# Performance work log

Hardware: AMD Instinct MI355X
Metric: run time of the kernel (lower is better)

Reference implementation:

```python
import jax, jax.numpy as jnp
import numpy as np

B, K, D, DH, GH = 4096, 16384, 512, 512, 32
MAX_ITER = 30
TOL = 1e-5

def setup_inputs() -> dict:
    key = jax.random.key(0)
    k = jax.random.split(key, 7)
    s = lambda fan: 1.0 / np.sqrt(fan)  # torch nn.Linear default init scale
    return {
        "query": jax.random.normal(k[0], (B, D), jnp.float32),
        "patterns": jax.random.normal(k[1], (K, D), jnp.float32),
        "Wq": jax.random.uniform(k[2], (D, DH), jnp.float32, -s(D), s(D)),
        "Wk": jax.random.uniform(k[3], (D, DH), jnp.float32, -s(D), s(D)),
        "Wv": jax.random.uniform(k[4], (D, D), jnp.float32, -s(D), s(D)),
        "log_beta": jnp.log(jnp.asarray(2.0, jnp.float32)),  # beta_init=2.0
        "g1_w": jax.random.uniform(k[5], (2 * D + 1, GH), jnp.float32, -s(2 * D + 1), s(2 * D + 1)),
        "g1_b": jnp.zeros((GH,), jnp.float32),
        "g2_w": jax.random.uniform(k[6], (GH, 1), jnp.float32, -s(GH), s(GH)),
        "g2_b": jnp.zeros((1,), jnp.float32),
    }

def _attn_step(z, Wq, k_projT, v_proj, beta):
    # z: (B, d) -> softmax(beta * (zWq)(KWk)^T) @ (KWv): (B, d)
    logits = beta * ((z @ Wq) @ k_projT)  # (B, K)
    return jax.nn.softmax(logits, axis=-1) @ v_proj

def reference(query, patterns, Wq, Wk, Wv, log_beta, g1_w, g1_b, g2_w, g2_b):
    beta = jnp.exp(log_beta)
    k_projT = (patterns @ Wk).T  # (dh, K)
    v_proj = patterns @ Wv       # (K, d)

    # shallow path: one attention step from the raw query
    out_shallow = _attn_step(query, Wq, k_projT, v_proj, beta)

    # deep path: fixed-point iteration z = f(z), z0 = out_shallow
    def cond(c):
        _, rel, it = c
        return (rel > TOL) & (it < MAX_ITER)

    def body(c):
        z, _, it = c
        z_new = _attn_step(z, Wq, k_projT, v_proj, beta)
        rel = jnp.linalg.norm(z_new - z) / (jnp.linalg.norm(z_new) + 1e-8)
        return z_new, rel, it + 1

    out_deep, _, _ = jax.lax.while_loop(cond, body, (out_shallow, jnp.float32(1.0), 0))

    # gate on [shallow, deep, ||shallow - deep||]
    div = jnp.linalg.norm(out_shallow - out_deep, axis=-1, keepdims=True)  # (B, 1)
    gate_in = jnp.concatenate([out_shallow, out_deep, div], axis=-1)       # (B, 2d+1)
    h = jax.nn.gelu(gate_in @ g1_w + g1_b, approximate=False)  # torch GELU is exact erf
    alpha = jax.nn.sigmoid(h @ g2_w + g2_b)                    # (B, 1)
    output = alpha * out_shallow + (1.0 - alpha) * out_deep
    return output, out_shallow, out_deep
```

## Files before the change

### kernel.cpp

```cpp
#include <hip/hip_runtime.h>
#include <hip/hip_bf16.h>
#include <math.h>

#define BROWS 4096
#define KPAT  16384
#define DDIM  512
#define NGRP  256
#define TOLF  1e-5f
#define KSEGS 8
#define KSEGLEN (KPAT / KSEGS)

typedef __attribute__((ext_vector_type(8))) short bf16x8;
typedef __attribute__((ext_vector_type(8))) _Float16 f16x8;
typedef __attribute__((ext_vector_type(4))) float f32x4;

typedef __attribute__((address_space(1))) const void gvoid_t;
typedef __attribute__((address_space(3))) void lvoid_t;
#define ASYNC_COPY16(g, l) \
  __builtin_amdgcn_global_load_lds((gvoid_t*)(g), (lvoid_t*)(l), 16, 0, 0)

#define SWZ_SCOL(lane) ((((lane) & 7) ^ (((lane) >> 3) & 7)) * 8)
#define SWZ_OFF(R, G)  (((R) * 64) + ((((G) ^ ((R) & 7))) * 8))

__device__ __forceinline__ unsigned short f2bf_rn(float x) {
  unsigned u = __float_as_uint(x);
  u = u + 0x7FFFu + ((u >> 16) & 1u);
  return (unsigned short)(u >> 16);
}
__device__ __forceinline__ unsigned short f2h_bits(float x) {
  union { _Float16 h; unsigned short u; } cv;
  cv.h = (_Float16)x;
  return cv.u;
}
__device__ __forceinline__ float h_bits2f(unsigned short u) {
  union { _Float16 h; unsigned short u; } cv;
  cv.u = u;
  return (float)cv.h;
}

__global__ void init_kernel(float* acc, int* flag) {
  acc[0] = 0.f; acc[1] = 0.f;
  acc[2] = 1e30f;
  *flag = 0;
}

__global__ void zero_out_kernel(float* p, int n, const int* __restrict__ flag) {
  if (flag && *(volatile const int*)flag) return;
  int i = blockIdx.x * 256 + threadIdx.x;
  if (i < n) p[i] = 0.f;
}

__global__ __launch_bounds__(256) void transpose_kernel(
    const float* __restrict__ in, void* __restrict__ outp,
    int R, int C, int ldO, int coff, int mode)
{
  __shared__ float tile[32][33];
  const int bx = blockIdx.x, by = blockIdx.y;
  const int tx = threadIdx.x & 31, ty = threadIdx.x >> 5;
  #pragma unroll
  for (int j = 0; j < 4; ++j) {
    int rr = by * 32 + ty + j * 8;
    tile[ty + j * 8][tx] = in[(long)rr * C + bx * 32 + tx];
  }
  __syncthreads();
  #pragma unroll
  for (int j = 0; j < 4; ++j) {
    int orow = bx * 32 + ty + j * 8;
    int ocol = by * 32 + tx;
    float v = tile[tx][ty + j * 8];
    if (mode == 2) ((unsigned short*)outp)[(long)orow * ldO + coff + ocol] = f2h_bits(v);
    else           ((float*)outp)[(long)orow * ldO + coff + ocol] = v;
  }
}

__global__ __launch_bounds__(256) void pack_split(
    const float* __restrict__ X, unsigned short* __restrict__ Y, int n)
{
  int i = blockIdx.x * 256 + threadIdx.x;
  if (i >= n) return;
  float x = X[i];
  unsigned u = __float_as_uint(x);
  unsigned short hi = (unsigned short)(u >> 16);
  float hif = __uint_as_float(u & 0xFFFF0000u);
  unsigned short lo = f2bf_rn(x - hif);
  int r = i >> 9, c = i & 511;
  Y[(long)r * 1024 + c] = hi;
  Y[(long)r * 1024 + 512 + c] = lo;
}

__global__ __launch_bounds__(256) void pack_f16(
    const float* __restrict__ X, unsigned short* __restrict__ Y, int n)
{
  int i = blockIdx.x * 256 + threadIdx.x;
  if (i >= n) return;
  Y[i] = f2h_bits(X[i]);
}

__global__ __launch_bounds__(256) void btgemm_setup(
    const unsigned short* __restrict__ A,
    const unsigned short* __restrict__ Bm,
    float* __restrict__ C, int ldC)
{
  __shared__ unsigned short As[128 * 64];
  __shared__ unsigned short Bs[128 * 64];
  const int tid = threadIdx.x;
  const int w = tid >> 6, lane = tid & 63;
  const int wm = w >> 1, wn = w & 1;
  const long mBase = (long)blockIdx.y * 128;
  const long nBase = (long)blockIdx.x * 128;

  f32x4 acc[4][4];
  const f32x4 zero4 = {0.f, 0.f, 0.f, 0.f};
  #pragma unroll
  for (int i = 0; i < 4; ++i)
    #pragma unroll
    for (int j = 0; j < 4; ++j) acc[i][j] = zero4;

  const int srow = w * 32 + (lane >> 3);
  const int scol = SWZ_SCOL(lane);
  const unsigned short* Ag = A + (mBase + srow) * 1024L + scol;
  const unsigned short* Bg = Bm + (nBase + srow) * 1024L + scol;
  unsigned short* AsW = As + w * 2048;
  unsigned short* BsW = Bs + w * 2048;
  const int lrow = lane & 15, lkq = lane >> 4;
  const int rx = lrow & 7;

  for (int k0 = 0; k0 < 1536; k0 += 64) {
    const int ak = (k0 < 512)  ? k0 : k0 - 512;
    const int bk = (k0 < 1024) ? k0 : k0 - 1024;
    __syncthreads();
    #pragma unroll
    for (int j = 0; j < 4; ++j) {
      ASYNC_COPY16(Ag + (long)j * 8 * 1024 + ak, AsW + j * 512);
      ASYNC_COPY16(Bg + (long)j * 8 * 1024 + bk, BsW + j * 512);
    }
    __syncthreads();
    #pragma unroll
    for (int s = 0; s < 2; ++s) {
      bf16x8 af[4], bfv[4];
      #pragma unroll
      for (int mi = 0; mi < 4; ++mi)
        af[mi] = *(const bf16x8*)(As + (wm * 64 + mi * 16 + lrow) * 64
                                     + (((s * 4 + lkq) ^ rx) * 8));
      #pragma unroll
      for (int ni = 0; ni < 4; ++ni)
        bfv[ni] = *(const bf16x8*)(Bs + (wn * 64 + ni * 16 + lrow) * 64
                                      + (((s * 4 + lkq) ^ rx) * 8));
      #pragma unroll
      for (int mi = 0; mi < 4; ++mi)
        #pragma unroll
        for (int ni = 0; ni < 4; ++ni)
          acc[mi][ni] = __builtin_amdgcn_mfma_f32_16x16x32_bf16(af[mi], bfv[ni], acc[mi][ni], 0, 0, 0);
    }
  }

  const int r0 = lkq * 4, cc = lrow;
  #pragma unroll
  for (int mi = 0; mi < 4; ++mi)
    #pragma unroll
    for (int r = 0; r < 4; ++r) {
      const long grow = mBase + wm * 64 + mi * 16 + r0 + r;
      #pragma unroll
      for (int ni = 0; ni < 4; ++ni) {
        const long gcol = nBase + wn * 64 + ni * 16 + cc;
        C[grow * ldC + gcol] = acc[mi][ni][r];
      }
    }
}

__global__ __launch_bounds__(256) void btgemm_exp(
    const unsigned short* __restrict__ A,
    const unsigned short* __restrict__ Bm,
    unsigned short* __restrict__ P,
    float* __restrict__ smax, float* __restrict__ ssum,
    const float* __restrict__ log_beta,
    const int* __restrict__ flag)
{
  if (flag && *(volatile const int*)flag) return;
  __shared__ unsigned short As[128 * 64];
  __shared__ unsigned short Bs[128 * 64];
  const float beta = __expf(log_beta[0]);
  const int tid = threadIdx.x;
  const int w = tid >> 6, lane = tid & 63;
  const int wm = w >> 1, wn = w & 1;
  const long mBase = (long)blockIdx.x * 128;
  const long nBase = (long)blockIdx.y * 128;

  f32x4 acc[4][4];
  const f32x4 zero4 = {0.f, 0.f, 0.f, 0.f};
  #pragma unroll
  for (int i = 0; i < 4; ++i)
    #pragma unroll
    for (int j = 0; j < 4; ++j) acc[i][j] = zero4;

  const int srow = w * 32 + (lane >> 3);
  const int scol = SWZ_SCOL(lane);
  const unsigned short* Ag = A + (mBase + srow) * 512L + scol;
  const unsigned short* Bg = Bm + (nBase + srow) * 512L + scol;
  unsigned short* AsW = As + w * 2048;
  unsigned short* BsW = Bs + w * 2048;
  const int lrow = lane & 15, lkq = lane >> 4;
  const int rx = lrow & 7;

  for (int k0 = 0; k0 < 512; k0 += 64) {
    __syncthreads();
    #pragma unroll
    for (int j = 0; j < 4; ++j) {
      ASYNC_COPY16(Ag + (long)j * 8 * 512 + k0, AsW + j * 512);
      ASYNC_COPY16(Bg + (long)j * 8 * 512 + k0, BsW + j * 512);
    }
    __syncthreads();
    #pragma unroll
    for (int s = 0; s < 2; ++s) {
      f16x8 af[4], bfv[4];
      #pragma unroll
      for (int mi = 0; mi < 4; ++mi)
        af[mi] = *(const f16x8*)(As + (wm * 64 + mi * 16 + lrow) * 64
                                    + (((s * 4 + lkq) ^ rx) * 8));
      #pragma unroll
      for (int ni = 0; ni < 4; ++ni)
        bfv[ni] = *(const f16x8*)(Bs + (wn * 64 + ni * 16 + lrow) * 64
                                     + (((s * 4 + lkq) ^ rx) * 8));
      #pragma unroll
      for (int mi = 0; mi < 4; ++mi)
        #pragma unroll
        for (int ni = 0; ni < 4; ++ni)
          acc[mi][ni] = __builtin_amdgcn_mfma_f32_16x16x32_f16(af[mi], bfv[ni], acc[mi][ni], 0, 0, 0);
    }
  }

  const int r0 = lkq * 4, cc = lrow;
  const int g = (int)(nBase >> 6) + wn;
  const long gbase = nBase + wn * 64;
  #pragma unroll
  for (int mi = 0; mi < 4; ++mi) {
    #pragma unroll
    for (int r = 0; r < 4; ++r) {
      const long grow = mBase + wm * 64 + mi * 16 + r0 + r;
      float rm = fmaxf(fmaxf(acc[mi][0][r], acc[mi][1][r]),
                       fmaxf(acc[mi][2][r], acc[mi][3][r]));
      #pragma unroll
      for (int off = 1; off < 16; off <<= 1)
        rm = fmaxf(rm, __shfl_xor(rm, off, 64));
      unsigned short pv[4];
      float se = 0.f;
      #pragma unroll
      for (int ni = 0; ni < 4; ++ni) {
        pv[ni] = f2h_bits(__expf(beta * (acc[mi][ni][r] - rm)));
        se += h_bits2f(pv[ni]);
      }
      #pragma unroll
      for (int ni = 0; ni < 4; ++ni)
        P[grow * KPAT + gbase + ni * 16 + cc] = pv[ni];
      #pragma unroll
      for (int off = 1; off < 16; off <<= 1)
        se += __shfl_xor(se, off, 64);
      if (cc == 0) {
        smax[grow * NGRP + g] = rm;
        ssum[grow * NGRP + g] = se;
      }
    }
  }
}

__global__ __launch_bounds__(256) void scale_kernel(
    const float* __restrict__ smax, const float* __restrict__ ssum,
    float* __restrict__ tvec, float* __restrict__ lbuf,
    const float* __restrict__ log_beta, const int* __restrict__ flag)
{
  if (flag && *(volatile const int*)flag) return;
  const int row = blockIdx.x, tid = threadIdx.x;
  const float beta = __expf(log_beta[0]);
  __shared__ float red[8];
  __shared__ float M_s;
  float m = smax[(long)row * NGRP + tid];
  float mm = m;
  #pragma unroll
  for (int off = 32; off >= 1; off >>= 1) mm = fmaxf(mm, __shfl_down(mm, off, 64));
  if ((tid & 63) == 0) red[tid >> 6] = mm;
  __syncthreads();
  if (tid == 0) M_s = fmaxf(fmaxf(red[0], red[1]), fmaxf(red[2], red[3]));
  __syncthreads();
  const float M = M_s;
  const float t = __expf(beta * (m - M));
  tvec[(long)row * NGRP + tid] = t;
  float lp = t * ssum[(long)row * NGRP + tid];
  #pragma unroll
  for (int off = 32; off >= 1; off >>= 1) lp += __shfl_down(lp, off, 64);
  if ((tid & 63) == 0) red[tid >> 6] = lp;
  __syncthreads();
  if (tid == 0) lbuf[row] = (red[0] + red[1]) + (red[2] + red[3]);
}

__global__ __launch_bounds__(256) void btgemm_splitk(
    const unsigned short* __restrict__ A,
    const unsigned short* __restrict__ Bm,
    const float* __restrict__ tvec,
    float* __restrict__ C,
    const int* __restrict__ flag)
{
  if (*(volatile const int*)flag) return;
  __shared__ unsigned short As[128 * 64];
  __shared__ unsigned short Bs[128 * 64];
  __shared__ float ts[128 * 33];
  const int tid = threadIdx.x;
  const int w = tid >> 6, lane = tid & 63;
  const int wm = w >> 1, wn = w & 1;
  const long mBase = (long)blockIdx.y * 128;
  const long nBase = (long)blockIdx.x * 128;
  const int kbase = blockIdx.z * KSEGLEN;
  const int g0 = kbase >> 6;

  for (int idx = tid; idx < 128 * 32; idx += 256) {
    int rr = idx >> 5, jj = idx & 31;
    ts[rr * 33 + jj] = tvec[(mBase + rr) * (long)NGRP + g0 + jj];
  }

  f32x4 acc[4][4];
  const f32x4 zero4 = {0.f, 0.f, 0.f, 0.f};
  #pragma unroll
  for (int i = 0; i < 4; ++i)
    #pragma unroll
    for (int j = 0; j < 4; ++j) acc[i][j] = zero4;

  const int srow = w * 32 + (lane >> 3);
  const int scol = SWZ_SCOL(lane);
  const unsigned short* Ag = A + (mBase + srow) * (long)KPAT + scol + kbase;
  const unsigned short* Bg = Bm + (nBase + srow) * (long)KPAT + scol + kbase;
  unsigned short* AsW = As + w * 2048;
  unsigned short* BsW = Bs + w * 2048;
  const int lrow = lane & 15, lkq = lane >> 4;
  const int rx = lrow & 7;

  for (int k0 = 0; k0 < KSEGLEN; k0 += 64) {
    __syncthreads();
    #pragma unroll
    for (int j = 0; j < 4; ++j) {
      ASYNC_COPY16(Ag + (long)j * 8 * KPAT + k0, AsW + j * 512);
      ASYNC_COPY16(Bg + (long)j * 8 * KPAT + k0, BsW + j * 512);
    }
    __syncthreads();
    const int jj = k0 >> 6;
    _Float16 th[4];
    #pragma unroll
    for (int mi = 0; mi < 4; ++mi)
      th[mi] = (_Float16)ts[(wm * 64 + mi * 16 + lrow) * 33 + jj];
    #pragma unroll
    for (int s = 0; s < 2; ++s) {
      f16x8 af[4], bfv[4];
      #pragma unroll
      for (int mi = 0; mi < 4; ++mi) {
        af[mi] = *(const f16x8*)(As + (wm * 64 + mi * 16 + lrow) * 64
                                    + (((s * 4 + lkq) ^ rx) * 8));
        f16x8 tv = {th[mi], th[mi], th[mi], th[mi], th[mi], th[mi], th[mi], th[mi]};
        af[mi] = af[mi] * tv;
      }
      #pragma unroll
      for (int ni = 0; ni < 4; ++ni)
        bfv[ni] = *(const f16x8*)(Bs + (wn * 64 + ni * 16 + lrow) * 64
                                     + (((s * 4 + lkq) ^ rx) * 8));
      #pragma unroll
      for (int mi = 0; mi < 4; ++mi)
        #pragma unroll
        for (int ni = 0; ni < 4; ++ni)
          acc[mi][ni] = __builtin_amdgcn_mfma_f32_16x16x32_f16(af[mi], bfv[ni], acc[mi][ni], 0, 0, 0);
    }
  }

  const int r0 = lkq * 4, cc = lrow;
  #pragma unroll
  for (int mi = 0; mi < 4; ++mi)
    #pragma unroll
    for (int r = 0; r < 4; ++r) {
      const long grow = mBase + wm * 64 + mi * 16 + r0 + r;
      #pragma unroll
      for (int ni = 0; ni < 4; ++ni) {
        const long gcol = nBase + wn * 64 + ni * 16 + cc;
        atomicAdd(&C[grow * DDIM + gcol], acc[mi][ni][r]);
      }
    }
}

__global__ __launch_bounds__(256) void reduce_commit(
    float4* __restrict__ zc, const float4* __restrict__ zn,
    unsigned short* __restrict__ zf16, const float* __restrict__ lvec,
    float* __restrict__ acc, const int* __restrict__ flag)
{
  if (*(volatile const int*)flag) return;
  const int tid = threadIdx.x;
  const int i = blockIdx.x * 256 + tid;
  const int row = i >> 7;
  const int c0 = (i & 127) * 4;
  const float rs = 1.0f / lvec[row];
  float4 a = zn[i];
  a.x *= rs; a.y *= rs; a.z *= rs; a.w *= rs;
  float4 b = zc[i];
  float dx = a.x - b.x, dy = a.y - b.y, dz = a.z - b.z, dw = a.w - b.w;
  float d2 = dx * dx + dy * dy + dz * dz + dw * dw;
  float n2 = a.x * a.x + a.y * a.y + a.z * a.z + a.w * a.w;
  zc[i] = a;
  *(ushort4*)(zf16 + (long)row * 512 + c0) =
      make_ushort4(f2h_bits(a.x), f2h_bits(a.y), f2h_bits(a.z), f2h_bits(a.w));

  __shared__ float rd[8], rn[8];
  #pragma unroll
  for (int off = 32; off >= 1; off >>= 1) {
    d2 += __shfl_down(d2, off, 64);
    n2 += __shfl_down(n2, off, 64);
  }
  if ((tid & 63) == 0) { rd[tid >> 6] = d2; rn[tid >> 6] = n2; }
  __syncthreads();
  if (tid == 0) {
    atomicAdd(acc,     (rd[0] + rd[1]) + (rd[2] + rd[3]));
    atomicAdd(acc + 1, (rn[0] + rn[1]) + (rn[2] + rn[3]));
  }
}

__global__ __launch_bounds__(256) void commit_shallow(
    float4* __restrict__ shal, float4* __restrict__ zc,
    const float4* __restrict__ zn, unsigned short* __restrict__ zf16,
    const float* __restrict__ lvec)
{
  const int i = blockIdx.x * 256 + threadIdx.x;
  const int row = i >> 7;
  const int c0 = (i & 127) * 4;
  const float rs = 1.0f / lvec[row];
  float4 a = zn[i];
  a.x *= rs; a.y *= rs; a.z *= rs; a.w *= rs;
  shal[i] = a; zc[i] = a;
  *(ushort4*)(zf16 + (long)row * 512 + c0) =
      make_ushort4(f2h_bits(a.x), f2h_bits(a.y), f2h_bits(a.z), f2h_bits(a.w));
}

__global__ void finalize_kernel(float* acc, int* flag) {
  if (*flag) return;
  float rel = sqrtf(acc[0]) / (sqrtf(acc[1]) + 1e-8f);
  float prev = acc[2];
  if (rel <= TOLF || (rel < 5e-3f && rel >= prev)) *flag = 1;
  acc[2] = rel;
  acc[0] = 0.f; acc[1] = 0.f;
}

__global__ __launch_bounds__(256) void epilogue_kernel(
    const float* __restrict__ shallow, const float* __restrict__ deep,
    const float* __restrict__ g1w, const float* __restrict__ g1b,
    const float* __restrict__ g2w, const float* __restrict__ g2b,
    float* __restrict__ out)
{
  const int r = blockIdx.x, tid = threadIdx.x;
  __shared__ float ss[512], sd[512], red[8], hred[8][32], hval[32];
  __shared__ float div_s, alpha_s;
  float dacc = 0.f;
  for (int c = tid; c < 512; c += 256) {
    float s = shallow[(long)r * 512 + c];
    float d = deep[(long)r * 512 + c];
    ss[c] = s; sd[c] = d;
    float df = s - d; dacc += df * df;
  }
  #pragma unroll
  for (int off = 32; off >= 1; off >>= 1) dacc += __shfl_down(dacc, off, 64);
  if ((tid & 63) == 0) red[tid >> 6] = dacc;
  __syncthreads();
  if (tid == 0) div_s = sqrtf((red[0] + red[1]) + (red[2] + red[3]));
  __syncthreads();
  const float dv = div_s;

  const int g = tid & 31, seg = tid >> 5;
  float p = 0.f;
  for (int jj = 0; jj < 64; ++jj) {
    int j = seg * 64 + jj;
    p += ss[j] * g1w[j * 32 + g] + sd[j] * g1w[(512 + j) * 32 + g];
  }
  hred[seg][g] = p;
  __syncthreads();
  if (tid < 32) {
    float h = g1b[tid] + dv * g1w[1024 * 32 + tid];
    #pragma unroll
    for (int sgi = 0; sgi < 8; ++sgi) h += hred[sgi][tid];
    float ge = 0.5f * h * (1.0f + erff(h * 0.70710678118f));
    hval[tid] = ge * g2w[tid];
  }
  __syncthreads();
  if (tid == 0) {
    float a = g2b[0];
    #pragma unroll
    for (int i = 0; i < 32; ++i) a += hval[i];
    alpha_s = 1.0f / (1.0f + expf(-a));
  }
  __syncthreads();
  const float al = alpha_s;
  const long BD = (long)BROWS * DDIM;
  for (int c = tid; c < 512; c += 256) {
    float s = ss[c], d = sd[c];
    out[(long)r * 512 + c]          = al * s + (1.f - al) * d;
    out[BD + (long)r * 512 + c]     = s;
    out[2 * BD + (long)r * 512 + c] = d;
  }
}

extern "C" void kernel_launch(void* const* d_in, const int* in_sizes, int n_in,
                              void* d_out, int out_size, void* d_ws, size_t ws_size,
                              hipStream_t stream)
{
  const float* query    = (const float*)d_in[0];
  const float* patterns = (const float*)d_in[1];
  const float* Wq       = (const float*)d_in[2];
  const float* Wk       = (const float*)d_in[3];
  const float* Wv       = (const float*)d_in[4];
  const float* log_beta = (const float*)d_in[5];
  const float* g1w      = (const float*)d_in[6];
  const float* g1b      = (const float*)d_in[7];
  const float* g2w      = (const float*)d_in[8];
  const float* g2b      = (const float*)d_in[9];
  float* out = (float*)d_out;

  char* base = (char*)d_ws;
  size_t off = 0;
  auto alloc = [&](size_t bytes) -> char* {
    char* p = base + off;
    off = (off + bytes + 255) & ~(size_t)255;
    return p;
  };
  unsigned short* At_f16 = (unsigned short*)alloc((size_t)KPAT * DDIM * 2);
  unsigned short* VPT    = (unsigned short*)alloc((size_t)DDIM * KPAT * 2);
  float* z_cur   = (float*)alloc((size_t)BROWS * DDIM * 4);
  float* z_new   = (float*)alloc((size_t)BROWS * DDIM * 4);
  float* shallow = (float*)alloc((size_t)BROWS * DDIM * 4);
  unsigned short* z_f16 = (unsigned short*)alloc((size_t)BROWS * DDIM * 2);
  float* Smax = (float*)alloc((size_t)BROWS * NGRP * 4);
  float* Ssum = (float*)alloc((size_t)BROWS * NGRP * 4);
  float* tvec = (float*)alloc((size_t)BROWS * NGRP * 4);
  float* lbuf = (float*)alloc((size_t)BROWS * 4);
  float* acc  = (float*)alloc(256);
  int* flag   = (int*)(acc + 8);
  char* scr = alloc(0);
  const size_t used = (size_t)(scr - base);
  const size_t scr_avail = (ws_size > used) ? ws_size - used : 0;

  const size_t MB = 1048576;
  const size_t MINSCR = 18 * MB;
  if (scr_avail < MINSCR) {
    zero_out_kernel<<<(out_size + 255) / 256, 256, 0, stream>>>(out, out_size, nullptr);
    return;
  }
  int c = 512;
  if      (scr_avail >= (size_t)4096 * KPAT * 2) c = 4096;
  else if (scr_avail >= (size_t)2048 * KPAT * 2) c = 2048;
  else if (scr_avail >= (size_t)1024 * KPAT * 2) c = 1024;
  const int nch = BROWS / c;

  unsigned short* P = (unsigned short*)scr;

  char* wscr = base + ((used + scr_avail - 7 * MB) & ~(size_t)255);
  unsigned short* Wk_pack  = (unsigned short*)(wscr + 0 * MB);
  unsigned short* Wq_pack  = (unsigned short*)(wscr + 1 * MB);
  unsigned short* W2T_pack = (unsigned short*)(wscr + 2 * MB);
  unsigned short* WvT_pack = (unsigned short*)(wscr + 3 * MB);
  float* W2f  = (float*)(wscr + 4 * MB);
  float* Wtmp = (float*)(wscr + 5 * MB);

  init_kernel<<<1, 1, 0, stream>>>(acc, flag);
  pack_split<<<1024, 256, 0, stream>>>(Wk, Wk_pack, 512 * 512);
  pack_split<<<1024, 256, 0, stream>>>(Wq, Wq_pack, 512 * 512);
  btgemm_setup<<<dim3(4, 4), 256, 0, stream>>>(Wk_pack, Wq_pack, W2f, 512);
  transpose_kernel<<<dim3(16, 16), 256, 0, stream>>>(W2f, Wtmp, 512, 512, 512, 0, 0);
  pack_split<<<1024, 256, 0, stream>>>(Wtmp, W2T_pack, 512 * 512);
  transpose_kernel<<<dim3(16, 16), 256, 0, stream>>>(Wv, Wtmp, 512, 512, 512, 0, 0);
  pack_split<<<1024, 256, 0, stream>>>(Wtmp, WvT_pack, 512 * 512);

  if (scr_avail >= 75 * MB) {
    unsigned short* pat_pack = (unsigned short*)scr;
    float* tmpf = (float*)(scr + (size_t)KPAT * 1024 * 2);
    pack_split<<<(KPAT * 512) / 256, 256, 0, stream>>>(patterns, pat_pack, KPAT * 512);
    btgemm_setup<<<dim3(4, KPAT / 128), 256, 0, stream>>>(pat_pack, WvT_pack, tmpf, 512);
    transpose_kernel<<<dim3(16, KPAT / 32), 256, 0, stream>>>(tmpf, VPT, KPAT, 512, KPAT, 0, 2);
    btgemm_setup<<<dim3(4, KPAT / 128), 256, 0, stream>>>(pat_pack, W2T_pack, tmpf, 512);
    pack_f16<<<(KPAT * 512) / 256, 256, 0, stream>>>(tmpf, At_f16, KPAT * 512);
  } else {
    const int pc = 1024;
    unsigned short* patc_pack = (unsigned short*)scr;
    float* tmpf = (float*)(scr + (size_t)pc * 1024 * 2);
    for (int pb = 0; pb < KPAT; pb += pc) {
      pack_split<<<pc * 2, 256, 0, stream>>>(patterns + (long)pb * 512, patc_pack, pc * 512);
      btgemm_setup<<<dim3(4, pc / 128), 256, 0, stream>>>(patc_pack, WvT_pack, tmpf, 512);
      transpose_kernel<<<dim3(16, pc / 32), 256, 0, stream>>>(tmpf, VPT, pc, 512, KPAT, pb, 2);
      btgemm_setup<<<dim3(4, pc / 128), 256, 0, stream>>>(patc_pack, W2T_pack, tmpf, 512);
      pack_f16<<<pc * 2, 256, 0, stream>>>(tmpf, At_f16 + (long)pb * 512, pc * 512);
    }
  }

  const int NZB = (BROWS * DDIM) / 256;
  const int NCB = (BROWS * DDIM / 4) / 256;

  pack_f16<<<8192, 256, 0, stream>>>(query, z_f16, BROWS * 512);
  zero_out_kernel<<<NZB, 256, 0, stream>>>(z_new, BROWS * DDIM, nullptr);
  for (int ch = 0; ch < nch; ++ch) {
    const long r0 = (long)ch * c;
    btgemm_exp<<<dim3(c / 128, 128), 256, 0, stream>>>(z_f16 + r0 * 512, At_f16, P,
                                                       Smax + r0 * NGRP, Ssum + r0 * NGRP,
                                                       log_beta, nullptr);
    scale_kernel<<<c, 256, 0, stream>>>(Smax + r0 * NGRP, Ssum + r0 * NGRP,
                                        tvec + r0 * NGRP, lbuf + r0, log_beta, nullptr);
    btgemm_splitk<<<dim3(4, c / 128, KSEGS), 256, 0, stream>>>(P, VPT, tvec + r0 * NGRP,
                                                               z_new + r0 * 512, flag);
  }
  commit_shallow<<<NCB, 256, 0, stream>>>((float4*)shallow, (float4*)z_cur,
                                          (const float4*)z_new, z_f16, lbuf);

  for (int it = 0; it < 30; ++it) {
    zero_out_kernel<<<NZB, 256, 0, stream>>>(z_new, BROWS * DDIM, flag);
    for (int ch = 0; ch < nch; ++ch) {
      const long r0 = (long)ch * c;
      btgemm_exp<<<dim3(c / 128, 128), 256, 0, stream>>>(z_f16 + r0 * 512, At_f16, P,
                                                         Smax + r0 * NGRP, Ssum + r0 * NGRP,
                                                         log_beta, flag);
      scale_kernel<<<c, 256, 0, stream>>>(Smax + r0 * NGRP, Ssum + r0 * NGRP,
                                          tvec + r0 * NGRP, lbuf + r0, log_beta, flag);
      btgemm_splitk<<<dim3(4, c / 128, KSEGS), 256, 0, stream>>>(P, VPT, tvec + r0 * NGRP,
                                                                 z_new + r0 * 512, flag);
    }
    reduce_commit<<<NCB, 256, 0, stream>>>((float4*)z_cur, (const float4*)z_new,
                                           z_f16, lbuf, acc, flag);
    finalize_kernel<<<1, 1, 0, stream>>>(acc, flag);
  }

  epilogue_kernel<<<BROWS, 256, 0, stream>>>(shallow, z_cur, g1w, g1b, g2w, g2b, out);
}
```

Measured before the change: 10.45 ms.

## Replace LDS staging with register double-buffered direct global loads in GEMMs

```diff
diff --git a/kernel.cpp b/kernel.cpp
--- a/kernel.cpp
+++ b/kernel.cpp
@@ -20,7 +20,8 @@
   __builtin_amdgcn_global_load_lds((gvoid_t*)(g), (lvoid_t*)(l), 16, 0, 0)
 
 #define SWZ_SCOL(lane) ((((lane) & 7) ^ (((lane) >> 3) & 7)) * 8)
-#define SWZ_OFF(R, G)  (((R) * 64) + ((((G) ^ ((R) & 7))) * 8))
+
+#define LD8(p) (*(const f16x8*)(p))
 
 __device__ __forceinline__ unsigned short f2bf_rn(float x) {
   unsigned u = __float_as_uint(x);
@@ -177,14 +178,16 @@
     const int* __restrict__ flag)
 {
   if (flag && *(volatile const int*)flag) return;
-  __shared__ unsigned short As[128 * 64];
-  __shared__ unsigned short Bs[128 * 64];
   const float beta = __expf(log_beta[0]);
   const int tid = threadIdx.x;
   const int w = tid >> 6, lane = tid & 63;
   const int wm = w >> 1, wn = w & 1;
   const long mBase = (long)blockIdx.x * 128;
   const long nBase = (long)blockIdx.y * 128;
+  const int lrow = lane & 15, lkq = lane >> 4;
+
+  const unsigned short* Ar = A + (mBase + wm * 64 + lrow) * 512L + lkq * 8;
+  const unsigned short* Br = Bm + (nBase + wn * 64 + lrow) * 512L + lkq * 8;
 
   f32x4 acc[4][4];
   const f32x4 zero4 = {0.f, 0.f, 0.f, 0.f};
@@ -193,39 +196,39 @@
     #pragma unroll
     for (int j = 0; j < 4; ++j) acc[i][j] = zero4;
 
-  const int srow = w * 32 + (lane >> 3);
-  const int scol = SWZ_SCOL(lane);
-  const unsigned short* Ag = A + (mBase + srow) * 512L + scol;
-  const unsigned short* Bg = Bm + (nBase + srow) * 512L + scol;
-  unsigned short* AsW = As + w * 2048;
-  unsigned short* BsW = Bs + w * 2048;
-  const int lrow = lane & 15, lkq = lane >> 4;
-  const int rx = lrow & 7;
-
-  for (int k0 = 0; k0 < 512; k0 += 64) {
-    __syncthreads();
-    #pragma unroll
-    for (int j = 0; j < 4; ++j) {
-      ASYNC_COPY16(Ag + (long)j * 8 * 512 + k0, AsW + j * 512);
-      ASYNC_COPY16(Bg + (long)j * 8 * 512 + k0, BsW + j * 512);
-    }
-    __syncthreads();
-    #pragma unroll
-    for (int s = 0; s < 2; ++s) {
-      f16x8 af[4], bfv[4];
-      #pragma unroll
-      for (int mi = 0; mi < 4; ++mi)
-        af[mi] = *(const f16x8*)(As + (wm * 64 + mi * 16 + lrow) * 64
-                                    + (((s * 4 + lkq) ^ rx) * 8));
+  f16x8 a0[4], b0[4], a1[4], b1[4];
+  #pragma unroll
+  for (int i = 0; i < 4; ++i) {
+    a0[i] = LD8(Ar + i * 8192);
+    b0[i] = LD8(Br + i * 8192);
+    a1[i] = LD8(Ar + i * 8192 + 32);
+    b1[i] = LD8(Br + i * 8192 + 32);
+  }
+  #pragma unroll
+  for (int kk = 0; kk < 512; kk += 64) {
+    #pragma unroll
+    for (int mi = 0; mi < 4; ++mi)
       #pragma unroll
       for (int ni = 0; ni < 4; ++ni)
-        bfv[ni] = *(const f16x8*)(Bs + (wn * 64 + ni * 16 + lrow) * 64
-                                     + (((s * 4 + lkq) ^ rx) * 8));
-      #pragma unroll
-      for (int mi = 0; mi < 4; ++mi)
-        #pragma unroll
-        for (int ni = 0; ni < 4; ++ni)
-          acc[mi][ni] = __builtin_amdgcn_mfma_f32_16x16x32_f16(af[mi], bfv[ni], acc[mi][ni], 0, 0, 0);
+        acc[mi][ni] = __builtin_amdgcn_mfma_f32_16x16x32_f16(a0[mi], b0[ni], acc[mi][ni], 0, 0, 0);
+    if (kk + 64 < 512) {
+      #pragma unroll
+      for (int i = 0; i < 4; ++i) {
+        a0[i] = LD8(Ar + i * 8192 + kk + 64);
+        b0[i] = LD8(Br + i * 8192 + kk + 64);
+      }
+    }
+    #pragma unroll
+    for (int mi = 0; mi < 4; ++mi)
+      #pragma unroll
+      for (int ni = 0; ni < 4; ++ni)
+        acc[mi][ni] = __builtin_amdgcn_mfma_f32_16x16x32_f16(a1[mi], b1[ni], acc[mi][ni], 0, 0, 0);
+    if (kk + 96 < 512) {
+      #pragma unroll
+      for (int i = 0; i < 4; ++i) {
+        a1[i] = LD8(Ar + i * 8192 + kk + 96);
+        b1[i] = LD8(Br + i * 8192 + kk + 96);
+      }
     }
   }
 
@@ -300,8 +303,6 @@
     const int* __restrict__ flag)
 {
   if (*(volatile const int*)flag) return;
-  __shared__ unsigned short As[128 * 64];
-  __shared__ unsigned short Bs[128 * 64];
   __shared__ float ts[128 * 33];
   const int tid = threadIdx.x;
   const int w = tid >> 6, lane = tid & 63;
@@ -310,11 +311,17 @@
   const long nBase = (long)blockIdx.x * 128;
   const int kbase = blockIdx.z * KSEGLEN;
   const int g0 = kbase >> 6;
+  const int lrow = lane & 15, lkq = lane >> 4;
 
   for (int idx = tid; idx < 128 * 32; idx += 256) {
     int rr = idx >> 5, jj = idx & 31;
     ts[rr * 33 + jj] = tvec[(mBase + rr) * (long)NGRP + g0 + jj];
   }
+  __syncthreads();
+
+  const unsigned short* Ar = A + (mBase + wm * 64 + lrow) * (long)KPAT + kbase + lkq * 8;
+  const unsigned short* Br = Bm + (nBase + wn * 64 + lrow) * (long)KPAT + kbase + lkq * 8;
+  const long AMI = 16L * KPAT;
 
   f32x4 acc[4][4];
   const f32x4 zero4 = {0.f, 0.f, 0.f, 0.f};
@@ -323,47 +330,51 @@
     #pragma unroll
     for (int j = 0; j < 4; ++j) acc[i][j] = zero4;
 
-  const int srow = w * 32 + (lane >> 3);
-  const int scol = SWZ_SCOL(lane);
-  const unsigned short* Ag = A + (mBase + srow) * (long)KPAT + scol + kbase;
-  const unsigned short* Bg = Bm + (nBase + srow) * (long)KPAT + scol + kbase;
-  unsigned short* AsW = As + w * 2048;
-  unsigned short* BsW = Bs + w * 2048;
-  const int lrow = lane & 15, lkq = lane >> 4;
-  const int rx = lrow & 7;
-
-  for (int k0 = 0; k0 < KSEGLEN; k0 += 64) {
-    __syncthreads();
-    #pragma unroll
-    for (int j = 0; j < 4; ++j) {
-      ASYNC_COPY16(Ag + (long)j * 8 * KPAT + k0, AsW + j * 512);
-      ASYNC_COPY16(Bg + (long)j * 8 * KPAT + k0, BsW + j * 512);
-    }
-    __syncthreads();
-    const int jj = k0 >> 6;
+  f16x8 a0[4], b0[4], a1[4], b1[4];
+  #pragma unroll
+  for (int i = 0; i < 4; ++i) {
+    a0[i] = LD8(Ar + i * AMI);
+    b0[i] = LD8(Br + i * AMI);
+    a1[i] = LD8(Ar + i * AMI + 32);
+    b1[i] = LD8(Br + i * AMI + 32);
+  }
+  const int tsrow = wm * 64 + lrow;
+
+  for (int kk = 0; kk < KSEGLEN; kk += 64) {
+    const int jj = kk >> 6;
     _Float16 th[4];
     #pragma unroll
     for (int mi = 0; mi < 4; ++mi)
-      th[mi] = (_Float16)ts[(wm * 64 + mi * 16 + lrow) * 33 + jj];
-    #pragma unroll
-    for (int s = 0; s < 2; ++s) {
-      f16x8 af[4], bfv[4];
-      #pragma unroll
-      for (int mi = 0; mi < 4; ++mi) {
-        af[mi] = *(const f16x8*)(As + (wm * 64 + mi * 16 + lrow) * 64
-                                    + (((s * 4 + lkq) ^ rx) * 8));
-        f16x8 tv = {th[mi], th[mi], th[mi], th[mi], th[mi], th[mi], th[mi], th[mi]};
-        af[mi] = af[mi] * tv;
-      }
+      th[mi] = (_Float16)ts[(tsrow + mi * 16) * 33 + jj];
+    #pragma unroll
+    for (int mi = 0; mi < 4; ++mi) {
+      f16x8 tv = {th[mi], th[mi], th[mi], th[mi], th[mi], th[mi], th[mi], th[mi]};
+      f16x8 as = a0[mi] * tv;
       #pragma unroll
       for (int ni = 0; ni < 4; ++ni)
-        bfv[ni] = *(const f16x8*)(Bs + (wn * 64 + ni * 16 + lrow) * 64
-                                     + (((s * 4 + lkq) ^ rx) * 8));
-      #pragma unroll
-      for (int mi = 0; mi < 4; ++mi)
-        #pragma unroll
-        for (int ni = 0; ni < 4; ++ni)
-          acc[mi][ni] = __builtin_amdgcn_mfma_f32_16x16x32_f16(af[mi], bfv[ni], acc[mi][ni], 0, 0, 0);
+        acc[mi][ni] = __builtin_amdgcn_mfma_f32_16x16x32_f16(as, b0[ni], acc[mi][ni], 0, 0, 0);
+    }
+    if (kk + 64 < KSEGLEN) {
+      #pragma unroll
+      for (int i = 0; i < 4; ++i) {
+        a0[i] = LD8(Ar + i * AMI + kk + 64);
+        b0[i] = LD8(Br + i * AMI + kk + 64);
+      }
+    }
+    #pragma unroll
+    for (int mi = 0; mi < 4; ++mi) {
+      f16x8 tv = {th[mi], th[mi], th[mi], th[mi], th[mi], th[mi], th[mi], th[mi]};
+      f16x8 as = a1[mi] * tv;
+      #pragma unroll
+      for (int ni = 0; ni < 4; ++ni)
+        acc[mi][ni] = __builtin_amdgcn_mfma_f32_16x16x32_f16(as, b1[ni], acc[mi][ni], 0, 0, 0);
+    }
+    if (kk + 96 < KSEGLEN) {
+      #pragma unroll
+      for (int i = 0; i < 4; ++i) {
+        a1[i] = LD8(Ar + i * AMI + kk + 96);
+        b1[i] = LD8(Br + i * AMI + kk + 96);
+      }
     }
   }
 
```

Measured after the change: 18.30 ms. +75.1%, slower.
